# Performance work log

Measured on AMD Instinct MI355X. Metric: run time of the kernel, lower is better.

## Reference

```python
import jax, jax.numpy as jnp
import numpy as np

V, BLOCK, D, H, L = 32000, 2048, 768, 12, 4
B, T = 2, 2048
HD = D // H
FF = 4 * D


def setup_inputs() -> dict:
    key = jax.random.key(0)
    ks = jax.random.split(key, 20)
    s = 0.02
    inp = {
        "idx": jax.random.randint(ks[0], (B, T), 0, V),
        "tok_emb": jax.random.normal(ks[1], (V, D), jnp.float32) * s,
        "pos_emb": jax.random.normal(ks[2], (BLOCK, D), jnp.float32) * s,
        # per-layer stacked params (leading dim L); linear weights stored [in, out]
        "ln1_w": jnp.ones((L, D), jnp.float32),
        "ln1_b": jnp.zeros((L, D), jnp.float32),
        "Wqkv": jax.random.normal(ks[3], (L, D, 3 * D), jnp.float32) * s,
        "bqkv": jnp.zeros((L, 3 * D), jnp.float32),
        "Wproj": jax.random.normal(ks[4], (L, D, D), jnp.float32) * s,
        "bproj": jnp.zeros((L, D), jnp.float32),
        "ln2_w": jnp.ones((L, D), jnp.float32),
        "ln2_b": jnp.zeros((L, D), jnp.float32),
        "Wfc": jax.random.normal(ks[5], (L, D, FF), jnp.float32) * s,
        "bfc": jnp.zeros((L, FF), jnp.float32),
        "Wfc2": jax.random.normal(ks[6], (L, FF, D), jnp.float32) * s,
        "bfc2": jnp.zeros((L, D), jnp.float32),
        "lnf_w": jnp.ones((D,), jnp.float32),
        "lnf_b": jnp.zeros((D,), jnp.float32),
    }
    return inp


def _layernorm(x, w, b, eps=1e-5):
    mu = jnp.mean(x, axis=-1, keepdims=True)
    var = jnp.var(x, axis=-1, keepdims=True)
    return (x - mu) * jax.lax.rsqrt(var + eps) * w + b


def _attn(x, Wqkv, bqkv, Wproj, bproj):
    b, t, c = x.shape
    qkv = x @ Wqkv + bqkv  # [B,T,3D]
    q, k, v = jnp.split(qkv, 3, axis=-1)
    q = q.reshape(b, t, H, HD)
    k = k.reshape(b, t, H, HD)
    v = v.reshape(b, t, H, HD)
    scale = 1.0 / np.sqrt(HD)
    att = jnp.einsum("bthd,bshd->bhts", q, k) * scale  # [B,H,T,T]
    causal = jnp.tril(jnp.ones((t, t), bool))
    att = jnp.where(causal[None, None], att, -jnp.inf)
    att = jax.nn.softmax(att, axis=-1)
    out = jnp.einsum("bhts,bshd->bthd", att, v).reshape(b, t, c)
    return out @ Wproj + bproj


def reference(idx, tok_emb, pos_emb, ln1_w, ln1_b, Wqkv, bqkv, Wproj, bproj,
              ln2_w, ln2_b, Wfc, bfc, Wfc2, bfc2, lnf_w, lnf_b):
    t = idx.shape[1]
    x = tok_emb[idx] + pos_emb[:t][None]  # [B,T,D]
    for l in range(L):
        h = _layernorm(x, ln1_w[l], ln1_b[l])
        x = x + _attn(h, Wqkv[l], bqkv[l], Wproj[l], bproj[l])
        h = _layernorm(x, ln2_w[l], ln2_b[l])
        h = jax.nn.gelu(h @ Wfc[l] + bfc[l], approximate=False) @ Wfc2[l] + bfc2[l]
        x = x + h
    x = _layernorm(x, lnf_w, lnf_b)
    return x @ tok_emb.T  # tied head, [B,T,V]
```

## Files before the change

### kernel.cpp

```cpp
#include <hip/hip_runtime.h>
#include <math.h>

#define VOCAB  32000
#define DMODEL 768
#define NHEAD  12
#define NLAYER 4
#define BATCH  2
#define SEQ    2048
#define HEADD  64
#define FFDIM  3072
#define MROWS  (BATCH*SEQ)

typedef __attribute__((ext_vector_type(8))) short bf16x8;
typedef __attribute__((ext_vector_type(4))) float f32x4;

__device__ __forceinline__ unsigned short f2bf(float f) {
    union { float f; unsigned u; } v; v.f = f;
    unsigned r = v.u + 0x7fffu + ((v.u >> 16) & 1u);
    return (unsigned short)(r >> 16);
}

__device__ __forceinline__ void async_lds16(const unsigned short* g, unsigned short* l) {
    __builtin_amdgcn_global_load_lds(
        (const __attribute__((address_space(1))) unsigned int*)(const void*)g,
        (__attribute__((address_space(3))) unsigned int*)(void*)l, 16, 0, 0);
}

__global__ void cvt_bf16_x4(const float* __restrict__ in, unsigned short* __restrict__ out, int n4) {
    int i = blockIdx.x * blockDim.x + threadIdx.x;
    if (i >= n4) return;
    float4 v = ((const float4*)in)[i];
    uint2 o;
    o.x = (unsigned)f2bf(v.x) | ((unsigned)f2bf(v.y) << 16);
    o.y = (unsigned)f2bf(v.z) | ((unsigned)f2bf(v.w) << 16);
    ((uint2*)out)[i] = o;
}

__global__ void transpose_cvt(const float* __restrict__ W, unsigned short* __restrict__ Wt,
                              int Kdim, int Ndim) {
    __shared__ float tile[32][33];
    int l  = blockIdx.z;
    int k0 = blockIdx.x * 32;
    int n0 = blockIdx.y * 32;
    const float* Wl = W + (size_t)l * Kdim * Ndim;
    unsigned short* Wtl = Wt + (size_t)l * Kdim * Ndim;
    int c = threadIdx.x & 31, r = threadIdx.x >> 5;
#pragma unroll
    for (int i = 0; i < 4; i++)
        tile[r + i * 8][c] = Wl[(size_t)(k0 + r + i * 8) * Ndim + n0 + c];
    __syncthreads();
#pragma unroll
    for (int i = 0; i < 4; i++)
        Wtl[(size_t)(n0 + r + i * 8) * Kdim + k0 + c] = f2bf(tile[c][r + i * 8]);
}

__global__ void embed_kernel(const int* __restrict__ idx, const float* __restrict__ tok,
                             const float* __restrict__ pos, float* __restrict__ x) {
    int row = blockIdx.x;
    int t = row & (SEQ - 1);
    int tr = idx[row];
    const float4* ts = (const float4*)(tok + (size_t)tr * DMODEL);
    const float4* ps = (const float4*)(pos + (size_t)t * DMODEL);
    float4* xs = (float4*)(x + (size_t)row * DMODEL);
    int i = threadIdx.x;
    float4 a = ts[i], b = ps[i];
    xs[i] = make_float4(a.x + b.x, a.y + b.y, a.z + b.z, a.w + b.w);
}

__global__ void layernorm_kernel(const float* __restrict__ x, const float* __restrict__ w,
                                 const float* __restrict__ b, unsigned short* __restrict__ out) {
    int row = blockIdx.x;
    const float* xr = x + (size_t)row * DMODEL;
    int t = threadIdx.x;
    float v0 = xr[t], v1 = xr[t + 256], v2 = xr[t + 512];
    float s = v0 + v1 + v2;
    float ss = v0 * v0 + v1 * v1 + v2 * v2;
#pragma unroll
    for (int off = 32; off >= 1; off >>= 1) {
        s  += __shfl_xor(s, off);
        ss += __shfl_xor(ss, off);
    }
    __shared__ float red[8];
    int wave = t >> 6, lane = t & 63;
    if (lane == 0) { red[wave] = s; red[wave + 4] = ss; }
    __syncthreads();
    s  = red[0] + red[1] + red[2] + red[3];
    ss = red[4] + red[5] + red[6] + red[7];
    float mu = s * (1.0f / DMODEL);
    float var = ss * (1.0f / DMODEL) - mu * mu;
    float rs = rsqrtf(var + 1e-5f);
    unsigned short* orow = out + (size_t)row * DMODEL;
    orow[t]       = f2bf((v0 - mu) * rs * w[t]       + b[t]);
    orow[t + 256] = f2bf((v1 - mu) * rs * w[t + 256] + b[t + 256]);
    orow[t + 512] = f2bf((v2 - mu) * rs * w[t + 512] + b[t + 512]);
}

template <bool GELU_, bool RESID_, bool OUTBF16_, bool BIAS_>
__global__ __launch_bounds__(256) void gemm_kernel(
    const unsigned short* __restrict__ A,
    const unsigned short* __restrict__ Bw,
    const float* __restrict__ bias,
    const float* resid,
    float* Cf, unsigned short* Cb,
    int Ndim, int Kdim) {
    const int bm = blockIdx.x * 128;
    const int bn = blockIdx.y * 128;
    __shared__ unsigned short As[128][32];
    __shared__ unsigned short Bs[128][32];
    int tid = threadIdx.x;
    int wave = tid >> 6, lane = tid & 63;
    int wm = (wave >> 1) * 64, wn = (wave & 1) * 64;
    int quad = lane >> 4, ln = lane & 15;
    int srow = lane >> 2;
    int scol = (lane & 3) * 8;
    f32x4 acc[4][4] = {};

    for (int k0 = 0; k0 < Kdim; k0 += 32) {
        __syncthreads();
#pragma unroll
        for (int i = 0; i < 2; i++) {
            int ch = (wave << 1) | i;
            async_lds16(A  + (size_t)(bm + ch * 16 + srow) * Kdim + k0 + scol, &As[ch * 16][0]);
            async_lds16(Bw + (size_t)(bn + ch * 16 + srow) * Kdim + k0 + scol, &Bs[ch * 16][0]);
        }
        __syncthreads();
        bf16x8 af[4], bfr[4];
#pragma unroll
        for (int tm = 0; tm < 4; tm++) af[tm]  = *(const bf16x8*)(&As[wm + tm * 16 + ln][quad * 8]);
#pragma unroll
        for (int tn = 0; tn < 4; tn++) bfr[tn] = *(const bf16x8*)(&Bs[wn + tn * 16 + ln][quad * 8]);
#pragma unroll
        for (int tm = 0; tm < 4; tm++)
#pragma unroll
            for (int tn = 0; tn < 4; tn++)
                acc[tm][tn] = __builtin_amdgcn_mfma_f32_16x16x32_bf16(af[tm], bfr[tn], acc[tm][tn], 0, 0, 0);
    }

#pragma unroll
    for (int tm = 0; tm < 4; tm++)
#pragma unroll
        for (int tn = 0; tn < 4; tn++)
#pragma unroll
            for (int r = 0; r < 4; r++) {
                int row = bm + wm + tm * 16 + quad * 4 + r;
                int col = bn + wn + tn * 16 + ln;
                float c = acc[tm][tn][r];
                if (BIAS_) c += bias[col];
                if (GELU_) c = 0.5f * c * (1.0f + erff(c * 0.70710678118654752f));
                if (RESID_) c += resid[(size_t)row * Ndim + col];
                if (OUTBF16_) Cb[(size_t)row * Ndim + col] = f2bf(c);
                else          Cf[(size_t)row * Ndim + col] = c;
            }
}

__device__ __forceinline__ void stage_Ax(const unsigned short* A, int Kdim, int bm,
                                         unsigned short (*slotA)[64], int half, int ktile,
                                         int w, int lrow, int scol) {
#pragma unroll
    for (int j = 0; j < 2; j++) {
        int row = j * 128 + half * 64 + w * 8;
        const unsigned short* src = A + (size_t)(bm + row + lrow) * Kdim + ktile * 64 + scol;
        async_lds16(src, &slotA[row][0]);
    }
}
__device__ __forceinline__ void stage_Bx(const unsigned short* Bw, int Kdim, int bn,
                                         unsigned short (*slotB)[64], int half, int ktile,
                                         int w, int lrow, int scol) {
#pragma unroll
    for (int j = 0; j < 2; j++) {
        int gb = j * 64 + w * 8;
        int row = (gb >> 5) * 64 + half * 32 + (gb & 31);
        const unsigned short* src = Bw + (size_t)(bn + row + lrow) * Kdim + ktile * 64 + scol;
        async_lds16(src, &slotB[row][0]);
    }
}

#define PHASE(QM, QN, STAGE_STMT, VM_STMT)                                            \
  { bf16x8 af[4][2], bfv[2][2];                                                        \
    const char* Ab = (const char*)&lds[s][0][0][0];                                    \
    const char* Bb = (const char*)&lds[s][1][0][0];                                    \
    _Pragma("unroll") for (int j = 0; j < 4; j++) {                                    \
      int row = wr * 128 + (QM) * 64 + j * 16 + ln;                                    \
      int rs = row * 128, sw = (row & 7) << 4;                                         \
      _Pragma("unroll") for (int ks = 0; ks < 2; ks++)                                 \
        af[j][ks] = *(const bf16x8*)(Ab + rs + ((ks * 64 + quad * 16) ^ sw));          \
    }                                                                                  \
    _Pragma("unroll") for (int jn = 0; jn < 2; jn++) {                                 \
      int row = wc * 64 + (QN) * 32 + jn * 16 + ln;                                    \
      int rs = row * 128, sw = (row & 7) << 4;                                         \
      _Pragma("unroll") for (int ks = 0; ks < 2; ks++)                                 \
        bfv[jn][ks] = *(const bf16x8*)(Bb + rs + ((ks * 64 + quad * 16) ^ sw));        \
    }                                                                                  \
    STAGE_STMT;                                                                        \
    VM_STMT;                                                                           \
    __builtin_amdgcn_s_barrier(); asm volatile("" ::: "memory");                       \
    asm volatile("s_waitcnt lgkmcnt(0)" ::: "memory");                                 \
    __builtin_amdgcn_s_setprio(1);                                                     \
    _Pragma("unroll") for (int j = 0; j < 4; j++)                                      \
    _Pragma("unroll") for (int jn = 0; jn < 2; jn++)                                   \
    _Pragma("unroll") for (int ks = 0; ks < 2; ks++)                                   \
      acc[(QM) * 4 + j][(QN) * 2 + jn] = __builtin_amdgcn_mfma_f32_16x16x32_bf16(      \
          af[j][ks], bfv[jn][ks], acc[(QM) * 4 + j][(QN) * 2 + jn], 0, 0, 0);          \
    __builtin_amdgcn_s_setprio(0);                                                     \
    __builtin_amdgcn_s_barrier(); asm volatile("" ::: "memory"); }

__global__ __launch_bounds__(512, 2) void gemm256_kernel(
    const unsigned short* __restrict__ A,
    const unsigned short* __restrict__ Bw,
    float* __restrict__ Cf, int Ndim, int Kdim) {
    const int bm = blockIdx.x * 256;
    const int bn = blockIdx.y * 256;
    __shared__ unsigned short lds[2][2][256][64];
    int tid = threadIdx.x;
    int w = tid >> 6, lane = tid & 63;
    int wr = w >> 2, wc = w & 3;
    int quad = lane >> 4, ln = lane & 15;
    int lrow = lane >> 3;
    int scol = ((lane & 7) ^ lrow) << 3;
    f32x4 acc[8][4] = {};
    const int NT = Kdim >> 6;

    stage_Ax(A,  Kdim, bm, lds[0][0], 0, 0, w, lrow, scol);
    stage_Bx(Bw, Kdim, bn, lds[0][1], 0, 0, w, lrow, scol);
    stage_Ax(A,  Kdim, bm, lds[0][0], 1, 0, w, lrow, scol);
    stage_Bx(Bw, Kdim, bn, lds[0][1], 1, 0, w, lrow, scol);
    stage_Ax(A,  Kdim, bm, lds[1][0], 0, 1, w, lrow, scol);
    stage_Bx(Bw, Kdim, bn, lds[1][1], 0, 1, w, lrow, scol);
    asm volatile("s_waitcnt vmcnt(8)" ::: "memory");
    __builtin_amdgcn_s_barrier(); asm volatile("" ::: "memory");

    for (int t = 0; t < NT; t++) {
        const int s = t & 1;
        unsigned short (*nA)[64] = lds[s ^ 1][0];
        unsigned short (*nB)[64] = lds[s ^ 1][1];
        unsigned short (*cA)[64] = lds[s][0];
        unsigned short (*cB)[64] = lds[s][1];
        const bool st1 = (t + 1 < NT), st2 = (t + 2 < NT);

        PHASE(0, 0,
              if (st1) stage_Ax(A, Kdim, bm, nA, 1, t + 1, w, lrow, scol),
              if (st1) asm volatile("s_waitcnt vmcnt(6)" ::: "memory"))
        PHASE(0, 1,
              if (st1) stage_Bx(Bw, Kdim, bn, nB, 1, t + 1, w, lrow, scol),
              if (st1) asm volatile("s_waitcnt vmcnt(10)" ::: "memory"))
        PHASE(1, 0,
              if (st2) stage_Ax(A, Kdim, bm, cA, 0, t + 2, w, lrow, scol), )
        PHASE(1, 1,
              if (st2) stage_Bx(Bw, Kdim, bn, cB, 0, t + 2, w, lrow, scol),
              if (st2) { asm volatile("s_waitcnt vmcnt(8)" ::: "memory"); }
              else if (t == NT - 2) { asm volatile("s_waitcnt vmcnt(0)" ::: "memory"); })
    }

#pragma unroll
    for (int mf = 0; mf < 8; mf++)
#pragma unroll
        for (int nf = 0; nf < 4; nf++)
#pragma unroll
            for (int r = 0; r < 4; r++) {
                int row = bm + wr * 128 + mf * 16 + quad * 4 + r;
                int col = bn + wc * 64 + nf * 16 + ln;
                Cf[(size_t)row * Ndim + col] = acc[mf][nf][r];
            }
}

__global__ __launch_bounds__(256) void attn_kernel(const unsigned short* __restrict__ qkv,
                                                   unsigned short* __restrict__ out) {
    int qtile = blockIdx.x;
    int bh = blockIdx.y;
    int b = bh / NHEAD, h = bh % NHEAD;
    int q0 = qtile * 128;
    const unsigned short* base = qkv + (size_t)b * SEQ * (3 * DMODEL);

    __shared__ unsigned short Qs[128][72];
    __shared__ unsigned short Ks[64][72];
    __shared__ unsigned short Vs[64][72];
    __shared__ unsigned short Ps[128][72];

    int tid = threadIdx.x, wave = tid >> 6, lane = tid & 63;
    int quad = lane >> 4, ln = lane & 15;

    for (int c = tid; c < 1024; c += 256) {
        int r = c >> 3, col = (c & 7) * 8;
        *(bf16x8*)(&Qs[r][col]) =
            *(const bf16x8*)(base + (size_t)(q0 + r) * (3 * DMODEL) + h * HEADD + col);
    }
    __syncthreads();

    bf16x8 qf[2][2];
#pragma unroll
    for (int tm = 0; tm < 2; tm++)
#pragma unroll
        for (int ks = 0; ks < 2; ks++)
            qf[tm][ks] = *(const bf16x8*)(&Qs[wave * 32 + tm * 16 + ln][ks * 32 + quad * 8]);

    f32x4 o[2][4] = {};
    float mst[8], lst[8];
#pragma unroll
    for (int i = 0; i < 8; i++) { mst[i] = -3.0e38f; lst[i] = 0.0f; }

    const float scale = 0.125f;
    int nkt = qtile * 2 + 2;

    for (int kt = 0; kt < nkt; kt++) {
        __syncthreads();
        for (int c = tid; c < 512; c += 256) {
            int r = c >> 3, col = (c & 7) * 8;
            *(bf16x8*)(&Ks[r][col]) =
                *(const bf16x8*)(base + (size_t)(kt * 64 + r) * (3 * DMODEL) + DMODEL + h * HEADD + col);
            union { bf16x8 v; unsigned short u[8]; } vv;
            vv.v = *(const bf16x8*)(base + (size_t)(kt * 64 + r) * (3 * DMODEL) + 2 * DMODEL + h * HEADD + col);
#pragma unroll
            for (int j = 0; j < 8; j++) Vs[col + j][r] = vv.u[j];
        }
        __syncthreads();

        f32x4 s[2][4];
#pragma unroll
        for (int tm = 0; tm < 2; tm++)
#pragma unroll
            for (int tn = 0; tn < 4; tn++) s[tm][tn] = (f32x4){0.f, 0.f, 0.f, 0.f};
        bf16x8 kf[4][2];
#pragma unroll
        for (int tn = 0; tn < 4; tn++)
#pragma unroll
            for (int ks = 0; ks < 2; ks++)
                kf[tn][ks] = *(const bf16x8*)(&Ks[tn * 16 + ln][ks * 32 + quad * 8]);
#pragma unroll
        for (int tm = 0; tm < 2; tm++)
#pragma unroll
            for (int tn = 0; tn < 4; tn++)
#pragma unroll
                for (int ks = 0; ks < 2; ks++)
                    s[tm][tn] = __builtin_amdgcn_mfma_f32_16x16x32_bf16(qf[tm][ks], kf[tn][ks], s[tm][tn], 0, 0, 0);

#pragma unroll
        for (int tm = 0; tm < 2; tm++)
#pragma unroll
            for (int tn = 0; tn < 4; tn++)
#pragma unroll
                for (int r = 0; r < 4; r++) {
                    int qi = q0 + wave * 32 + tm * 16 + quad * 4 + r;
                    int kj = kt * 64 + tn * 16 + ln;
                    float sv = s[tm][tn][r] * scale;
                    s[tm][tn][r] = (kj > qi) ? -3.0e38f : sv;
                }

#pragma unroll
        for (int tm = 0; tm < 2; tm++)
#pragma unroll
            for (int r = 0; r < 4; r++) {
                float mx = fmaxf(fmaxf(s[tm][0][r], s[tm][1][r]), fmaxf(s[tm][2][r], s[tm][3][r]));
#pragma unroll
                for (int msk = 1; msk <= 8; msk <<= 1) mx = fmaxf(mx, __shfl_xor(mx, msk));
                int ri = tm * 4 + r;
                float mnew = fmaxf(mst[ri], mx);
                float alpha = __expf(mst[ri] - mnew);
                mst[ri] = mnew;
                float psum = 0.f;
#pragma unroll
                for (int tn = 0; tn < 4; tn++) {
                    float p = __expf(s[tm][tn][r] - mnew);
                    s[tm][tn][r] = p;
                    psum += p;
                }
#pragma unroll
                for (int msk = 1; msk <= 8; msk <<= 1) psum += __shfl_xor(psum, msk);
                lst[ri] = lst[ri] * alpha + psum;
#pragma unroll
                for (int nd = 0; nd < 4; nd++) o[tm][nd][r] *= alpha;
            }

#pragma unroll
        for (int tm = 0; tm < 2; tm++)
#pragma unroll
            for (int tn = 0; tn < 4; tn++)
#pragma unroll
                for (int r = 0; r < 4; r++)
                    Ps[wave * 32 + tm * 16 + quad * 4 + r][tn * 16 + ln] = f2bf(s[tm][tn][r]);

        bf16x8 pf[2][2], vf[4][2];
#pragma unroll
        for (int tm = 0; tm < 2; tm++)
#pragma unroll
            for (int ks = 0; ks < 2; ks++)
                pf[tm][ks] = *(const bf16x8*)(&Ps[wave * 32 + tm * 16 + ln][ks * 32 + quad * 8]);
#pragma unroll
        for (int nd = 0; nd < 4; nd++)
#pragma unroll
            for (int ks = 0; ks < 2; ks++)
                vf[nd][ks] = *(const bf16x8*)(&Vs[nd * 16 + ln][ks * 32 + quad * 8]);
#pragma unroll
        for (int tm = 0; tm < 2; tm++)
#pragma unroll
            for (int nd = 0; nd < 4; nd++)
#pragma unroll
                for (int ks = 0; ks < 2; ks++)
                    o[tm][nd] = __builtin_amdgcn_mfma_f32_16x16x32_bf16(pf[tm][ks], vf[nd][ks], o[tm][nd], 0, 0, 0);
    }

#pragma unroll
    for (int tm = 0; tm < 2; tm++)
#pragma unroll
        for (int r = 0; r < 4; r++) {
            float inv = 1.0f / lst[tm * 4 + r];
            int trow = q0 + wave * 32 + tm * 16 + quad * 4 + r;
#pragma unroll
            for (int nd = 0; nd < 4; nd++) {
                int col = h * HEADD + nd * 16 + ln;
                out[(size_t)(b * SEQ + trow) * DMODEL + col] = f2bf(o[tm][nd][r] * inv);
            }
        }
}

extern "C" void kernel_launch(void* const* d_in, const int* in_sizes, int n_in,
                              void* d_out, int out_size, void* d_ws, size_t ws_size,
                              hipStream_t stream) {
    const int*   idx   = (const int*)  d_in[0];
    const float* tok   = (const float*)d_in[1];
    const float* pos   = (const float*)d_in[2];
    const float* ln1w  = (const float*)d_in[3];
    const float* ln1b  = (const float*)d_in[4];
    const float* Wqkv  = (const float*)d_in[5];
    const float* bqkv  = (const float*)d_in[6];
    const float* Wproj = (const float*)d_in[7];
    const float* bproj = (const float*)d_in[8];
    const float* ln2w  = (const float*)d_in[9];
    const float* ln2b  = (const float*)d_in[10];
    const float* Wfc   = (const float*)d_in[11];
    const float* bfc   = (const float*)d_in[12];
    const float* Wfc2  = (const float*)d_in[13];
    const float* bfc2  = (const float*)d_in[14];
    const float* lnfw  = (const float*)d_in[15];
    const float* lnfb  = (const float*)d_in[16];

    char* ob = (char*)d_out;
    unsigned short* qkvb   = (unsigned short*)(ob + 0);
    float*          x      = (float*)(ob + 18874368);
    unsigned short* ffact  = (unsigned short*)(ob + 31457280);
    unsigned short* attnb  = (unsigned short*)(ob + 56623104);
    unsigned short* WqkvT  = (unsigned short*)(ob + 62914560);
    unsigned short* WprojT = (unsigned short*)(ob + 77070336);
    unsigned short* WfcT   = (unsigned short*)(ob + 81788928);
    unsigned short* Wfc2T  = (unsigned short*)(ob + 100663296);
    unsigned short* tokT   = (unsigned short*)d_ws;
    unsigned short* lnout  = (unsigned short*)((char*)d_ws + 49152000);

    cvt_bf16_x4<<<24000, 256, 0, stream>>>(tok, tokT, VOCAB * DMODEL / 4);
    transpose_cvt<<<dim3(24, 72, NLAYER), 256, 0, stream>>>(Wqkv,  WqkvT,  DMODEL, 3 * DMODEL);
    transpose_cvt<<<dim3(24, 24, NLAYER), 256, 0, stream>>>(Wproj, WprojT, DMODEL, DMODEL);
    transpose_cvt<<<dim3(24, 96, NLAYER), 256, 0, stream>>>(Wfc,   WfcT,   DMODEL, FFDIM);
    transpose_cvt<<<dim3(96, 24, NLAYER), 256, 0, stream>>>(Wfc2,  Wfc2T,  FFDIM,  DMODEL);

    embed_kernel<<<MROWS, 192, 0, stream>>>(idx, tok, pos, x);

    for (int l = 0; l < NLAYER; l++) {
        layernorm_kernel<<<MROWS, 256, 0, stream>>>(x, ln1w + l * DMODEL, ln1b + l * DMODEL, lnout);
        gemm_kernel<false, false, true, true><<<dim3(32, 18), 256, 0, stream>>>(
            lnout, WqkvT + (size_t)l * 3 * DMODEL * DMODEL, bqkv + l * 3 * DMODEL,
            nullptr, nullptr, qkvb, 3 * DMODEL, DMODEL);
        attn_kernel<<<dim3(16, BATCH * NHEAD), 256, 0, stream>>>(qkvb, attnb);
        gemm_kernel<false, true, false, true><<<dim3(32, 6), 256, 0, stream>>>(
            attnb, WprojT + (size_t)l * DMODEL * DMODEL, bproj + l * DMODEL,
            x, x, nullptr, DMODEL, DMODEL);
        layernorm_kernel<<<MROWS, 256, 0, stream>>>(x, ln2w + l * DMODEL, ln2b + l * DMODEL, lnout);
        gemm_kernel<true, false, true, true><<<dim3(32, 24), 256, 0, stream>>>(
            lnout, WfcT + (size_t)l * FFDIM * DMODEL, bfc + l * FFDIM,
            nullptr, nullptr, ffact, FFDIM, DMODEL);
        gemm_kernel<false, true, false, true><<<dim3(32, 6), 256, 0, stream>>>(
            ffact, Wfc2T + (size_t)l * FFDIM * DMODEL, bfc2 + l * DMODEL,
            x, x, nullptr, DMODEL, FFDIM);
    }

    layernorm_kernel<<<MROWS, 256, 0, stream>>>(x, lnfw, lnfb, lnout);
    gemm256_kernel<<<dim3(16, 125), 512, 0, stream>>>(lnout, tokT, (float*)d_out, VOCAB, DMODEL);
}
```

Before: 2.244 ms.

## Split attention query tile across 8 waves, reverse tile order, skip mask off-diagonal

The attention kernel now runs 512 threads per block, with each wave owning 16 query rows instead of 32. This halves per-wave register state and doubles the number of waves sharing each K/V tile load. Query tiles are issued in reverse order so the longest causal tiles start first, which helps load balance. The causal mask is now applied only on diagonal key tiles, with plain scaling elsewhere. Each K/V tile gives less MFMA work per wave, and the LDS loads and barriers are shared by more waves.

```diff
diff --git a/kernel.cpp b/kernel.cpp
--- a/kernel.cpp
+++ b/kernel.cpp
@@ -263,9 +263,9 @@
             }
 }
 
-__global__ __launch_bounds__(256) void attn_kernel(const unsigned short* __restrict__ qkv,
-                                                   unsigned short* __restrict__ out) {
-    int qtile = blockIdx.x;
+__global__ __launch_bounds__(512, 2) void attn_kernel(const unsigned short* __restrict__ qkv,
+                                                      unsigned short* __restrict__ out) {
+    int qtile = 15 - blockIdx.x;
     int bh = blockIdx.y;
     int b = bh / NHEAD, h = bh % NHEAD;
     int q0 = qtile * 128;
@@ -279,31 +279,30 @@
     int tid = threadIdx.x, wave = tid >> 6, lane = tid & 63;
     int quad = lane >> 4, ln = lane & 15;
 
-    for (int c = tid; c < 1024; c += 256) {
+    for (int c = tid; c < 1024; c += 512) {
         int r = c >> 3, col = (c & 7) * 8;
         *(bf16x8*)(&Qs[r][col]) =
             *(const bf16x8*)(base + (size_t)(q0 + r) * (3 * DMODEL) + h * HEADD + col);
     }
     __syncthreads();
 
-    bf16x8 qf[2][2];
-#pragma unroll
-    for (int tm = 0; tm < 2; tm++)
-#pragma unroll
-        for (int ks = 0; ks < 2; ks++)
-            qf[tm][ks] = *(const bf16x8*)(&Qs[wave * 32 + tm * 16 + ln][ks * 32 + quad * 8]);
-
-    f32x4 o[2][4] = {};
-    float mst[8], lst[8];
-#pragma unroll
-    for (int i = 0; i < 8; i++) { mst[i] = -3.0e38f; lst[i] = 0.0f; }
+    bf16x8 qf[2];
+#pragma unroll
+    for (int ks = 0; ks < 2; ks++)
+        qf[ks] = *(const bf16x8*)(&Qs[wave * 16 + ln][ks * 32 + quad * 8]);
+
+    f32x4 o[4] = {};
+    float mst[4], lst[4];
+#pragma unroll
+    for (int i = 0; i < 4; i++) { mst[i] = -3.0e38f; lst[i] = 0.0f; }
 
     const float scale = 0.125f;
     int nkt = qtile * 2 + 2;
 
     for (int kt = 0; kt < nkt; kt++) {
         __syncthreads();
-        for (int c = tid; c < 512; c += 256) {
+        {
+            int c = tid;
             int r = c >> 3, col = (c & 7) * 8;
             *(bf16x8*)(&Ks[r][col]) =
                 *(const bf16x8*)(base + (size_t)(kt * 64 + r) * (3 * DMODEL) + DMODEL + h * HEADD + col);
@@ -314,11 +313,9 @@
         }
         __syncthreads();
 
-        f32x4 s[2][4];
-#pragma unroll
-        for (int tm = 0; tm < 2; tm++)
-#pragma unroll
-            for (int tn = 0; tn < 4; tn++) s[tm][tn] = (f32x4){0.f, 0.f, 0.f, 0.f};
+        f32x4 s[4];
+#pragma unroll
+        for (int tn = 0; tn < 4; tn++) s[tn] = (f32x4){0.f, 0.f, 0.f, 0.f};
         bf16x8 kf[4][2];
 #pragma unroll
         for (int tn = 0; tn < 4; tn++)
@@ -326,90 +323,82 @@
             for (int ks = 0; ks < 2; ks++)
                 kf[tn][ks] = *(const bf16x8*)(&Ks[tn * 16 + ln][ks * 32 + quad * 8]);
 #pragma unroll
-        for (int tm = 0; tm < 2; tm++)
+        for (int tn = 0; tn < 4; tn++)
+#pragma unroll
+            for (int ks = 0; ks < 2; ks++)
+                s[tn] = __builtin_amdgcn_mfma_f32_16x16x32_bf16(qf[ks], kf[tn][ks], s[tn], 0, 0, 0);
+
+        if (kt >= qtile * 2) {
 #pragma unroll
             for (int tn = 0; tn < 4; tn++)
 #pragma unroll
-                for (int ks = 0; ks < 2; ks++)
-                    s[tm][tn] = __builtin_amdgcn_mfma_f32_16x16x32_bf16(qf[tm][ks], kf[tn][ks], s[tm][tn], 0, 0, 0);
-
-#pragma unroll
-        for (int tm = 0; tm < 2; tm++)
+                for (int r = 0; r < 4; r++) {
+                    int qi = q0 + wave * 16 + quad * 4 + r;
+                    int kj = kt * 64 + tn * 16 + ln;
+                    float sv = s[tn][r] * scale;
+                    s[tn][r] = (kj > qi) ? -3.0e38f : sv;
+                }
+        } else {
 #pragma unroll
             for (int tn = 0; tn < 4; tn++)
 #pragma unroll
-                for (int r = 0; r < 4; r++) {
-                    int qi = q0 + wave * 32 + tm * 16 + quad * 4 + r;
-                    int kj = kt * 64 + tn * 16 + ln;
-                    float sv = s[tm][tn][r] * scale;
-                    s[tm][tn][r] = (kj > qi) ? -3.0e38f : sv;
-                }
-
-#pragma unroll
-        for (int tm = 0; tm < 2; tm++)
-#pragma unroll
-            for (int r = 0; r < 4; r++) {
-                float mx = fmaxf(fmaxf(s[tm][0][r], s[tm][1][r]), fmaxf(s[tm][2][r], s[tm][3][r]));
-#pragma unroll
-                for (int msk = 1; msk <= 8; msk <<= 1) mx = fmaxf(mx, __shfl_xor(mx, msk));
-                int ri = tm * 4 + r;
-                float mnew = fmaxf(mst[ri], mx);
-                float alpha = __expf(mst[ri] - mnew);
-                mst[ri] = mnew;
-                float psum = 0.f;
-#pragma unroll
-                for (int tn = 0; tn < 4; tn++) {
-                    float p = __expf(s[tm][tn][r] - mnew);
-                    s[tm][tn][r] = p;
-                    psum += p;
-                }
-#pragma unroll
-                for (int msk = 1; msk <= 8; msk <<= 1) psum += __shfl_xor(psum, msk);
-                lst[ri] = lst[ri] * alpha + psum;
-#pragma unroll
-                for (int nd = 0; nd < 4; nd++) o[tm][nd][r] *= alpha;
+                for (int r = 0; r < 4; r++) s[tn][r] *= scale;
+        }
+
+#pragma unroll
+        for (int r = 0; r < 4; r++) {
+            float mx = fmaxf(fmaxf(s[0][r], s[1][r]), fmaxf(s[2][r], s[3][r]));
+#pragma unroll
+            for (int msk = 1; msk <= 8; msk <<= 1) mx = fmaxf(mx, __shfl_xor(mx, msk));
+            float mnew = fmaxf(mst[r], mx);
+            float alpha = __expf(mst[r] - mnew);
+            mst[r] = mnew;
+            float psum = 0.f;
+#pragma unroll
+            for (int tn = 0; tn < 4; tn++) {
+                float p = __expf(s[tn][r] - mnew);
+                s[tn][r] = p;
+                psum += p;
             }
-
-#pragma unroll
-        for (int tm = 0; tm < 2; tm++)
-#pragma unroll
-            for (int tn = 0; tn < 4; tn++)
-#pragma unroll
-                for (int r = 0; r < 4; r++)
-                    Ps[wave * 32 + tm * 16 + quad * 4 + r][tn * 16 + ln] = f2bf(s[tm][tn][r]);
-
-        bf16x8 pf[2][2], vf[4][2];
-#pragma unroll
-        for (int tm = 0; tm < 2; tm++)
-#pragma unroll
-            for (int ks = 0; ks < 2; ks++)
-                pf[tm][ks] = *(const bf16x8*)(&Ps[wave * 32 + tm * 16 + ln][ks * 32 + quad * 8]);
+#pragma unroll
+            for (int msk = 1; msk <= 8; msk <<= 1) psum += __shfl_xor(psum, msk);
+            lst[r] = lst[r] * alpha + psum;
+#pragma unroll
+            for (int nd = 0; nd < 4; nd++) o[nd][r] *= alpha;
+        }
+
+#pragma unroll
+        for (int tn = 0; tn < 4; tn++)
+#pragma unroll
+            for (int r = 0; r < 4; r++)
+                Ps[wave * 16 + quad * 4 + r][tn * 16 + ln] = f2bf(s[tn][r]);
+
+        bf16x8 pf[2], vf[4][2];
+#pragma unroll
+        for (int ks = 0; ks < 2; ks++)
+            pf[ks] = *(const bf16x8*)(&Ps[wave * 16 + ln][ks * 32 + quad * 8]);
 #pragma unroll
         for (int nd = 0; nd < 4; nd++)
 #pragma unroll
             for (int ks = 0; ks < 2; ks++)
                 vf[nd][ks] = *(const bf16x8*)(&Vs[nd * 16 + ln][ks * 32 + quad * 8]);
 #pragma unroll
-        for (int tm = 0; tm < 2; tm++)
-#pragma unroll
-            for (int nd = 0; nd < 4; nd++)
-#pragma unroll
-                for (int ks = 0; ks < 2; ks++)
-                    o[tm][nd] = __builtin_amdgcn_mfma_f32_16x16x32_bf16(pf[tm][ks], vf[nd][ks], o[tm][nd], 0, 0, 0);
-    }
-
-#pragma unroll
-    for (int tm = 0; tm < 2; tm++)
-#pragma unroll
-        for (int r = 0; r < 4; r++) {
-            float inv = 1.0f / lst[tm * 4 + r];
-            int trow = q0 + wave * 32 + tm * 16 + quad * 4 + r;
-#pragma unroll
-            for (int nd = 0; nd < 4; nd++) {
-                int col = h * HEADD + nd * 16 + ln;
-                out[(size_t)(b * SEQ + trow) * DMODEL + col] = f2bf(o[tm][nd][r] * inv);
-            }
+        for (int nd = 0; nd < 4; nd++)
+#pragma unroll
+            for (int ks = 0; ks < 2; ks++)
+                o[nd] = __builtin_amdgcn_mfma_f32_16x16x32_bf16(pf[ks], vf[nd][ks], o[nd], 0, 0, 0);
+    }
+
+#pragma unroll
+    for (int r = 0; r < 4; r++) {
+        float inv = 1.0f / lst[r];
+        int trow = q0 + wave * 16 + quad * 4 + r;
+#pragma unroll
+        for (int nd = 0; nd < 4; nd++) {
+            int col = h * HEADD + nd * 16 + ln;
+            out[(size_t)(b * SEQ + trow) * DMODEL + col] = f2bf(o[nd][r] * inv);
         }
+    }
 }
 
 extern "C" void kernel_launch(void* const* d_in, const int* in_sizes, int n_in,
@@ -458,7 +447,7 @@
         gemm_kernel<false, false, true, true><<<dim3(32, 18), 256, 0, stream>>>(
             lnout, WqkvT + (size_t)l * 3 * DMODEL * DMODEL, bqkv + l * 3 * DMODEL,
             nullptr, nullptr, qkvb, 3 * DMODEL, DMODEL);
-        attn_kernel<<<dim3(16, BATCH * NHEAD), 256, 0, stream>>>(qkvb, attnb);
+        attn_kernel<<<dim3(16, BATCH * NHEAD), 512, 0, stream>>>(qkvb, attnb);
         gemm_kernel<false, true, false, true><<<dim3(32, 6), 256, 0, stream>>>(
             attnb, WprojT + (size_t)l * DMODEL * DMODEL, bproj + l * DMODEL,
             x, x, nullptr, DMODEL, DMODEL);
```

Result: faster. 2.173 ms (-3.2%).
